# Kernel optimization log

Hardware: AMD Instinct MI355X
Metric: run time of the kernel (lower is better)

Reference implementation:

```python
import jax, jax.numpy as jnp
import numpy as np

N, E, G = 40000, 400000, 40
DIN, DH, DOUT = 128, 256, 128
NEG_SLOPE = 0.2  # PyG GATConv default leaky_relu slope


def _gat_layer(h_in, src, dst, W, a_src, a_dst, b, num_nodes):
    # h_in: [N, din]; src/dst: [E'] (self loops included); W: [din, dout]
    h = h_in @ W                                   # [N, dout]
    al_s = h @ a_src                               # [N]
    al_d = h @ a_dst                               # [N]
    e = jax.nn.leaky_relu(al_s[src] + al_d[dst], NEG_SLOPE)  # [E']
    # scatter-softmax over incoming edges of each dst node (stable)
    m = jax.ops.segment_max(e, dst, num_segments=num_nodes)
    ex = jnp.exp(e - m[dst])
    denom = jax.ops.segment_sum(ex, dst, num_segments=num_nodes)
    alpha = ex / denom[dst]                        # [E']
    out = jax.ops.segment_sum(h[src] * alpha[:, None], dst, num_segments=num_nodes)
    return out + b


def setup_inputs() -> dict:
    key = jax.random.key(0)
    ks = jax.random.split(key, 16)
    x = jax.random.normal(ks[0], (N, DIN), dtype=jnp.float32)
    edge_index = jax.random.randint(ks[1], (2, E), 0, N, dtype=jnp.int64)

    def lin(k, din, dout):
        return jax.random.normal(k, (din, dout), dtype=jnp.float32) / np.sqrt(din)

    def vec(k, d):
        return jax.random.normal(k, (d,), dtype=jnp.float32) / np.sqrt(d)

    return dict(
        x=x, edge_index=edge_index, num_graphs=G,
        W1=lin(ks[2], DIN, DH), a_src1=vec(ks[3], DH), a_dst1=vec(ks[4], DH), b1=jnp.zeros((DH,), jnp.float32),
        W2=lin(ks[5], DH, DH), a_src2=vec(ks[6], DH), a_dst2=vec(ks[7], DH), b2=jnp.zeros((DH,), jnp.float32),
        W3=lin(ks[8], DH, DOUT), a_src3=vec(ks[9], DOUT), a_dst3=vec(ks[10], DOUT), b3=jnp.zeros((DOUT,), jnp.float32),
    )


def reference(x, edge_index, num_graphs, W1, a_src1, a_dst1, b1, W2, a_src2, a_dst2, b2, W3, a_src3, a_dst3, b3):
    num_nodes = x.shape[0]
    # PyG GATConv adds self-loops by default
    loop = jnp.arange(num_nodes, dtype=edge_index.dtype)
    src = jnp.concatenate([edge_index[0], loop])
    dst = jnp.concatenate([edge_index[1], loop])

    h = jax.nn.relu(_gat_layer(x, src, dst, W1, a_src1, a_dst1, b1, num_nodes))
    # dropout is identity in eval mode
    h = jax.nn.relu(_gat_layer(h, src, dst, W2, a_src2, a_dst2, b2, num_nodes))
    h = _gat_layer(h, src, dst, W3, a_src3, a_dst3, b3, num_nodes)
    return h.reshape(num_graphs, num_nodes // num_graphs, -1)
```

## Files before the change

### kernel.cpp

```cpp
#include <hip/hip_runtime.h>
#include <hip/hip_bf16.h>
#include <type_traits>

typedef __attribute__((ext_vector_type(8))) short short8;
typedef __attribute__((ext_vector_type(4))) float f32x4;
typedef __attribute__((ext_vector_type(8))) unsigned short u16x8;

static __device__ __forceinline__ unsigned short f2b(float f) {
    unsigned int v = __float_as_uint(f);
    unsigned int r = (v + 0x7FFFu + ((v >> 16) & 1u)) >> 16;
    return (unsigned short)r;
}
static __device__ __forceinline__ float b2f(unsigned short u) {
    return __uint_as_float(((unsigned int)u) << 16);
}

__global__ void k_pre(const float* __restrict__ w1, unsigned short* __restrict__ t1,
                      const float* __restrict__ w2, unsigned short* __restrict__ t2,
                      const float* __restrict__ w3, unsigned short* __restrict__ t3,
                      int K1, int N1, int K2, int N2, int K3, int N3,
                      const int* __restrict__ dst, int* __restrict__ cnt, int E, int tblk) {
    if ((int)blockIdx.x < tblk) {
        int i = blockIdx.x * 256 + threadIdx.x;
        int n1 = K1 * N1, n2 = K2 * N2, n3 = K3 * N3;
        if (i < n1) {
            int k = i / N1, n = i % N1;
            t1[n * K1 + k] = f2b(w1[i]);
        } else if (i < n1 + n2) {
            int j = i - n1, k = j / N2, n = j % N2;
            t2[n * K2 + k] = f2b(w2[j]);
        } else if (i < n1 + n2 + n3) {
            int j = i - n1 - n2, k = j / N3, n = j % N3;
            t3[n * K3 + k] = f2b(w3[j]);
        }
    } else {
        int e = (blockIdx.x - tblk) * 256 + threadIdx.x;
        if (e < E) atomicAdd(&cnt[dst[e]], 1);
    }
}

__global__ void k_assign(const int* __restrict__ cnt, int* __restrict__ begptr,
                         int* __restrict__ colidx, int* __restrict__ fill,
                         int* __restrict__ cursor, int n) {
    int i = blockIdx.x * 256 + threadIdx.x;
    int lane = threadIdx.x & 63;
    int c = (i < n) ? cnt[i] + 1 : 0;
    int s = c;
#pragma unroll
    for (int off = 1; off < 64; off <<= 1) {
        int v = __shfl_up(s, off);
        if (lane >= off) s += v;
    }
    int wavesum = __shfl(s, 63);
    int base = 0;
    if (lane == 63) base = atomicAdd(cursor, wavesum);
    base = __shfl(base, 63);
    int beg = base + s - c;
    if (i < n) { begptr[i] = beg; colidx[beg] = i; fill[i] = beg + 1; }
}

template<int NC, typename AT>
static __device__ __forceinline__ void gemm_body(const AT* __restrict__ A,
                                                 const unsigned short* __restrict__ Bt,
                                                 unsigned short* __restrict__ H,
                                                 const float* __restrict__ asrc,
                                                 const float* __restrict__ adst,
                                                 float* __restrict__ als,
                                                 float* __restrict__ ald,
                                                 int K, int blk) {
    __shared__ unsigned short As[64][72];
    __shared__ unsigned short Bs[NC][72];
    __shared__ float sps[64], spd[64];
    const int tid  = threadIdx.x;
    const int lane = tid & 63;
    const int wv   = tid >> 6;
    const int rowBase = blk * 64;
    const int quad = lane >> 4;
    const int l16  = lane & 15;
    constexpr int CG = NC / 32;
    const int wrow = (wv & 1) * 32;
    const int wcol = (wv >> 1) * (NC / 2);
    f32x4 acc[2][CG] = {};

    if (tid < 64) { sps[tid] = 0.f; spd[tid] = 0.f; }

    const int ar = tid >> 2;
    const int ak = (tid & 3) * 16;

    for (int kk = 0; kk < K; kk += 64) {
        if constexpr (std::is_same_v<AT, float>) {
            const float* ap = A + (size_t)(rowBase + ar) * K + kk + ak;
            f32x4 a0 = *(const f32x4*)ap;
            f32x4 a1 = *(const f32x4*)(ap + 4);
            f32x4 a2 = *(const f32x4*)(ap + 8);
            f32x4 a3 = *(const f32x4*)(ap + 12);
            short8 s0, s1;
#pragma unroll
            for (int v = 0; v < 4; v++) {
                s0[v] = (short)f2b(a0[v]); s0[4 + v] = (short)f2b(a1[v]);
                s1[v] = (short)f2b(a2[v]); s1[4 + v] = (short)f2b(a3[v]);
            }
            *(short8*)&As[ar][ak] = s0;
            *(short8*)&As[ar][ak + 8] = s1;
        } else {
            const unsigned short* ap = A + (size_t)(rowBase + ar) * K + kk + ak;
            *(short8*)&As[ar][ak]     = *(const short8*)ap;
            *(short8*)&As[ar][ak + 8] = *(const short8*)(ap + 8);
        }
#pragma unroll
        for (int c = tid; c < NC * 4; c += 256) {
            int br = c >> 2, bk = (c & 3) * 16;
            const unsigned short* bp = Bt + (size_t)br * K + kk + bk;
            *(short8*)&Bs[br][bk]     = *(const short8*)bp;
            *(short8*)&Bs[br][bk + 8] = *(const short8*)(bp + 8);
        }
        __syncthreads();
#pragma unroll
        for (int s = 0; s < 2; s++) {
            short8 af0 = *(const short8*)&As[wrow + l16][s * 32 + quad * 8];
            short8 af1 = *(const short8*)&As[wrow + 16 + l16][s * 32 + quad * 8];
#pragma unroll
            for (int cg = 0; cg < CG; cg++) {
                short8 bf = *(const short8*)&Bs[wcol + cg * 16 + l16][s * 32 + quad * 8];
                acc[0][cg] = __builtin_amdgcn_mfma_f32_16x16x32_bf16(af0, bf, acc[0][cg], 0, 0, 0);
                acc[1][cg] = __builtin_amdgcn_mfma_f32_16x16x32_bf16(af1, bf, acc[1][cg], 0, 0, 0);
            }
        }
        __syncthreads();
    }

    float avs[CG], avd[CG];
#pragma unroll
    for (int cg = 0; cg < CG; cg++) {
        int gcol = wcol + cg * 16 + l16;
        avs[cg] = asrc[gcol];
        avd[cg] = adst[gcol];
#pragma unroll
        for (int rg = 0; rg < 2; rg++)
#pragma unroll
            for (int r = 0; r < 4; r++) {
                int grow = rowBase + wrow + rg * 16 + quad * 4 + r;
                H[(size_t)grow * NC + gcol] = f2b(acc[rg][cg][r]);
            }
    }
#pragma unroll
    for (int rg = 0; rg < 2; rg++)
#pragma unroll
        for (int r = 0; r < 4; r++) {
            float ps = 0.f, pd = 0.f;
#pragma unroll
            for (int cg = 0; cg < CG; cg++) { ps += acc[rg][cg][r] * avs[cg]; pd += acc[rg][cg][r] * avd[cg]; }
#pragma unroll
            for (int off = 8; off; off >>= 1) { ps += __shfl_xor(ps, off); pd += __shfl_xor(pd, off); }
            if (l16 == 0) {
                int lrow = wrow + rg * 16 + quad * 4 + r;
                atomicAdd(&sps[lrow], ps);
                atomicAdd(&spd[lrow], pd);
            }
        }
    __syncthreads();
    if (tid < 64) { als[rowBase + tid] = sps[tid]; ald[rowBase + tid] = spd[tid]; }
}

template<int NC, typename AT>
__global__ __launch_bounds__(256) void k_gemm(const AT* __restrict__ A,
                                              const unsigned short* __restrict__ Bt,
                                              unsigned short* __restrict__ H,
                                              const float* __restrict__ asrc,
                                              const float* __restrict__ adst,
                                              float* __restrict__ als,
                                              float* __restrict__ ald, int K) {
    gemm_body<NC, AT>(A, Bt, H, asrc, adst, als, ald, K, blockIdx.x);
}

template<int NC, typename AT>
__global__ __launch_bounds__(256) void k_gemm_scatter(const AT* __restrict__ A,
                                                      const unsigned short* __restrict__ Bt,
                                                      unsigned short* __restrict__ H,
                                                      const float* __restrict__ asrc,
                                                      const float* __restrict__ adst,
                                                      float* __restrict__ als,
                                                      float* __restrict__ ald, int K, int gblk,
                                                      const int* __restrict__ src,
                                                      const int* __restrict__ dst,
                                                      int* __restrict__ fill,
                                                      int* __restrict__ colidx, int E) {
    if ((int)blockIdx.x < gblk) {
        gemm_body<NC, AT>(A, Bt, H, asrc, adst, als, ald, K, blockIdx.x);
    } else {
        int e = (blockIdx.x - gblk) * 256 + threadIdx.x;
        if (e < E) {
            int s = src[e], d = dst[e];
            int pos = atomicAdd(&fill[d], 1);
            colidx[pos] = s;
        }
    }
}

template<int DOUT, bool RELU, typename OutT>
__global__ __launch_bounds__(256) void k_edge(const unsigned short* __restrict__ h,
                                              const float* __restrict__ als,
                                              const float* __restrict__ ald,
                                              const int* __restrict__ begptr,
                                              const int* __restrict__ cnt,
                                              const int* __restrict__ colidx,
                                              const float* __restrict__ bias,
                                              OutT* __restrict__ out, int N) {
    int node = blockIdx.x * 4 + (threadIdx.x >> 6);
    if (node >= N) return;
    int lane = threadIdx.x & 63;
    int beg = begptr[node];
    int deg = cnt[node] + 1;
    float aldi = ald[node];

    float ex_lane = 0.f;
    int   s_lane = 0;
    float dsum = 0.f;
    for (int j = lane; j < deg; j += 64) {
        int s = colidx[beg + j];
        float e = als[s] + aldi;
        e = e > 0.f ? e : 0.2f * e;
        float ex = __expf(e);
        if (j < 64) { ex_lane = ex; s_lane = s; }
        dsum += ex;
    }
#pragma unroll
    for (int off = 32; off; off >>= 1) dsum += __shfl_xor(dsum, off);
    float inv = 1.0f / dsum;
    float w_lane = ex_lane * inv;

    constexpr int QV  = DOUT / 16;
    constexpr int NC8 = QV / 8;
    const int l16g    = lane & 15;
    const int quarter = lane >> 4;
    const size_t dimOff = (size_t)l16g * QV;
    float acc[QV] = {};
    int lim = deg < 64 ? deg : 64;
    for (int t = 0; 4 * t < lim; t++) {
        int idx = 4 * t + quarter;
        float wj = __shfl(w_lane, idx);
        int   sj = __shfl(s_lane, idx);
        const unsigned short* hp = h + (size_t)sj * DOUT + dimOff;
        u16x8 c[NC8];
#pragma unroll
        for (int u = 0; u < NC8; u++) c[u] = *(const u16x8*)(hp + 8 * u);
#pragma unroll
        for (int u = 0; u < NC8; u++)
#pragma unroll
            for (int v = 0; v < 8; v++) acc[8 * u + v] += wj * b2f(c[u][v]);
    }
    for (int j = 64; j < deg; j++) {
        int sj = colidx[beg + j];
        float e = als[sj] + aldi;
        e = e > 0.f ? e : 0.2f * e;
        float wj = __expf(e) * inv;
        if (quarter == 0) {
            const unsigned short* hp = h + (size_t)sj * DOUT + dimOff;
#pragma unroll
            for (int u = 0; u < NC8; u++) {
                u16x8 c = *(const u16x8*)(hp + 8 * u);
#pragma unroll
                for (int v = 0; v < 8; v++) acc[8 * u + v] += wj * b2f(c[v]);
            }
        }
    }
#pragma unroll
    for (int v = 0; v < QV; v++) {
        acc[v] += __shfl_xor(acc[v], 16);
        acc[v] += __shfl_xor(acc[v], 32);
    }

    if (quarter == 0) {
        if constexpr (std::is_same_v<OutT, float>) {
            float* op = out + (size_t)node * DOUT + dimOff;
#pragma unroll
            for (int u = 0; u < QV / 4; u++) {
                f32x4 bv = *(const f32x4*)(bias + dimOff + 4 * u);
                f32x4 ov;
#pragma unroll
                for (int v = 0; v < 4; v++) {
                    float val = acc[4 * u + v] + bv[v];
                    if (RELU) val = fmaxf(val, 0.f);
                    ov[v] = val;
                }
                *(f32x4*)(op + 4 * u) = ov;
            }
        } else {
            unsigned short* op = out + (size_t)node * DOUT + dimOff;
#pragma unroll
            for (int u = 0; u < NC8; u++) {
                u16x8 ov;
#pragma unroll
                for (int v = 0; v < 8; v++) {
                    float val = acc[8 * u + v] + bias[dimOff + 8 * u + v];
                    if (RELU) val = fmaxf(val, 0.f);
                    ov[v] = f2b(val);
                }
                *(u16x8*)(op + 8 * u) = ov;
            }
        }
    }
}

extern "C" void kernel_launch(void* const* d_in, const int* in_sizes, int n_in,
                              void* d_out, int out_size, void* d_ws, size_t ws_size,
                              hipStream_t stream) {
    const int DIN = 128, DH = 256, DOUT = 128;
    const int N = in_sizes[0] / DIN;
    const int E = in_sizes[1] / 2;

    const float* x   = (const float*)d_in[0];
    const int*   ei  = (const int*)d_in[1];
    const float* W1  = (const float*)d_in[3];
    const float* as1 = (const float*)d_in[4];
    const float* ad1 = (const float*)d_in[5];
    const float* b1  = (const float*)d_in[6];
    const float* W2  = (const float*)d_in[7];
    const float* as2 = (const float*)d_in[8];
    const float* ad2 = (const float*)d_in[9];
    const float* b2  = (const float*)d_in[10];
    const float* W3  = (const float*)d_in[11];
    const float* as3 = (const float*)d_in[12];
    const float* ad3 = (const float*)d_in[13];
    const float* b3  = (const float*)d_in[14];
    float* outp = (float*)d_out;

    char* ws = (char*)d_ws;
    size_t off = 0;
    auto carve = [&](size_t bytes) { char* p = ws + off; off = (off + bytes + 255) & ~(size_t)255; return p; };
    unsigned short* hbuf = (unsigned short*)carve((size_t)N * DH * 2);
    unsigned short* gbuf = (unsigned short*)carve((size_t)N * DH * 2);
    float* als  = (float*)carve((size_t)N * 4);
    float* ald  = (float*)carve((size_t)N * 4);
    unsigned short* wt1 = (unsigned short*)carve((size_t)DIN * DH * 2);
    unsigned short* wt2 = (unsigned short*)carve((size_t)DH * DH * 2);
    unsigned short* wt3 = (unsigned short*)carve((size_t)DH * DOUT * 2);
    int* cnt    = (int*)carve((size_t)N * 4);
    int* cursor = (int*)carve(256);
    int* begptr = (int*)carve((size_t)N * 4);
    int* fill   = (int*)carve((size_t)N * 4);
    int* colidx = (int*)carve((size_t)(E + N) * 4);
    (void)ws_size; (void)n_in; (void)out_size;

    const int* e_src = ei;
    const int* e_dst = ei + E;

    hipMemsetAsync(cnt, 0, (size_t)((char*)cursor - (char*)cnt) + 4, stream);

    const int tot   = DIN * DH + DH * DH + DH * DOUT;
    const int tblk  = (tot + 255) / 256;
    const int eblk  = (E + 255) / 256;
    const int nblk4 = (N + 3) / 4;
    const int mblk  = N / 64;

    k_pre<<<tblk + eblk, 256, 0, stream>>>(W1, wt1, W2, wt2, W3, wt3,
                                           DIN, DH, DH, DH, DH, DOUT,
                                           e_dst, cnt, E, tblk);
    k_assign<<<(N + 255) / 256, 256, 0, stream>>>(cnt, begptr, colidx, fill, cursor, N);

    k_gemm_scatter<256, float><<<mblk + eblk, 256, 0, stream>>>(
        x, wt1, hbuf, as1, ad1, als, ald, DIN, mblk,
        e_src, e_dst, fill, colidx, E);
    k_edge<256, true, unsigned short><<<nblk4, 256, 0, stream>>>(hbuf, als, ald, begptr, cnt, colidx, b1, gbuf, N);

    k_gemm<256, unsigned short><<<mblk, 256, 0, stream>>>(gbuf, wt2, hbuf, as2, ad2, als, ald, DH);
    k_edge<256, true, unsigned short><<<nblk4, 256, 0, stream>>>(hbuf, als, ald, begptr, cnt, colidx, b2, gbuf, N);

    k_gemm<128, unsigned short><<<mblk, 256, 0, stream>>>(gbuf, wt3, hbuf, as3, ad3, als, ald, DH);
    k_edge<128, false, float><<<nblk4, 256, 0, stream>>>(hbuf, als, ald, begptr, cnt, colidx, b3, outp, N);
}
```

Before: 292.6 us.

## Map one node per 16-lane group in GAT edge aggregation kernel

```diff
diff --git a/kernel.cpp b/kernel.cpp
--- a/kernel.cpp
+++ b/kernel.cpp
@@ -206,55 +206,64 @@
                                               const int* __restrict__ colidx,
                                               const float* __restrict__ bias,
                                               OutT* __restrict__ out, int N) {
-    int node = blockIdx.x * 4 + (threadIdx.x >> 6);
+    int node = blockIdx.x * 16 + (threadIdx.x >> 4);
     if (node >= N) return;
-    int lane = threadIdx.x & 63;
+    int lane  = threadIdx.x & 63;
+    int l16   = lane & 15;
+    int qbase = lane & 48;
     int beg = begptr[node];
     int deg = cnt[node] + 1;
     float aldi = ald[node];
 
     float ex_lane = 0.f;
-    int   s_lane = 0;
+    int   s_lane  = 0;
     float dsum = 0.f;
-    for (int j = lane; j < deg; j += 64) {
+    for (int j = l16; j < deg; j += 16) {
         int s = colidx[beg + j];
         float e = als[s] + aldi;
         e = e > 0.f ? e : 0.2f * e;
         float ex = __expf(e);
-        if (j < 64) { ex_lane = ex; s_lane = s; }
+        if (j < 16) { ex_lane = ex; s_lane = s; }
         dsum += ex;
     }
 #pragma unroll
-    for (int off = 32; off; off >>= 1) dsum += __shfl_xor(dsum, off);
+    for (int off = 8; off; off >>= 1) dsum += __shfl_xor(dsum, off, 16);
     float inv = 1.0f / dsum;
     float w_lane = ex_lane * inv;
 
+    int d16 = deg < 16 ? deg : 16;
+    int m16 = d16;
+    m16 = max(m16, __shfl_xor(m16, 16));
+    m16 = max(m16, __shfl_xor(m16, 32));
+    int mall = deg;
+    mall = max(mall, __shfl_xor(mall, 16));
+    mall = max(mall, __shfl_xor(mall, 32));
+
     constexpr int QV  = DOUT / 16;
     constexpr int NC8 = QV / 8;
-    const int l16g    = lane & 15;
-    const int quarter = lane >> 4;
-    const size_t dimOff = (size_t)l16g * QV;
+    const size_t dimOff = (size_t)l16 * QV;
     float acc[QV] = {};
-    int lim = deg < 64 ? deg : 64;
-    for (int t = 0; 4 * t < lim; t++) {
-        int idx = 4 * t + quarter;
-        float wj = __shfl(w_lane, idx);
-        int   sj = __shfl(s_lane, idx);
-        const unsigned short* hp = h + (size_t)sj * DOUT + dimOff;
-        u16x8 c[NC8];
-#pragma unroll
-        for (int u = 0; u < NC8; u++) c[u] = *(const u16x8*)(hp + 8 * u);
-#pragma unroll
-        for (int u = 0; u < NC8; u++)
-#pragma unroll
-            for (int v = 0; v < 8; v++) acc[8 * u + v] += wj * b2f(c[u][v]);
-    }
-    for (int j = 64; j < deg; j++) {
-        int sj = colidx[beg + j];
-        float e = als[sj] + aldi;
-        e = e > 0.f ? e : 0.2f * e;
-        float wj = __expf(e) * inv;
-        if (quarter == 0) {
+
+    for (int t = 0; t < m16; t++) {
+        float wj = __shfl(w_lane, qbase + t);
+        int   sj = __shfl(s_lane, qbase + t);
+        if (wj != 0.f) {
+            const unsigned short* hp = h + (size_t)sj * DOUT + dimOff;
+            u16x8 c[NC8];
+#pragma unroll
+            for (int u = 0; u < NC8; u++) c[u] = *(const u16x8*)(hp + 8 * u);
+#pragma unroll
+            for (int u = 0; u < NC8; u++)
+#pragma unroll
+                for (int v = 0; v < 8; v++) acc[8 * u + v] += wj * b2f(c[u][v]);
+        }
+    }
+    for (int t = 16; t < mall; t++) {
+        if (t < deg) {
+            int sj = colidx[beg + t];
+            float e = als[sj] + aldi;
+            e = e > 0.f ? e : 0.2f * e;
+            float wj = __expf(e) * inv;
             const unsigned short* hp = h + (size_t)sj * DOUT + dimOff;
 #pragma unroll
             for (int u = 0; u < NC8; u++) {
@@ -264,40 +273,33 @@
             }
         }
     }
-#pragma unroll
-    for (int v = 0; v < QV; v++) {
-        acc[v] += __shfl_xor(acc[v], 16);
-        acc[v] += __shfl_xor(acc[v], 32);
-    }
-
-    if (quarter == 0) {
-        if constexpr (std::is_same_v<OutT, float>) {
-            float* op = out + (size_t)node * DOUT + dimOff;
-#pragma unroll
-            for (int u = 0; u < QV / 4; u++) {
-                f32x4 bv = *(const f32x4*)(bias + dimOff + 4 * u);
-                f32x4 ov;
-#pragma unroll
-                for (int v = 0; v < 4; v++) {
-                    float val = acc[4 * u + v] + bv[v];
-                    if (RELU) val = fmaxf(val, 0.f);
-                    ov[v] = val;
-                }
-                *(f32x4*)(op + 4 * u) = ov;
-            }
-        } else {
-            unsigned short* op = out + (size_t)node * DOUT + dimOff;
-#pragma unroll
-            for (int u = 0; u < NC8; u++) {
-                u16x8 ov;
-#pragma unroll
-                for (int v = 0; v < 8; v++) {
-                    float val = acc[8 * u + v] + bias[dimOff + 8 * u + v];
-                    if (RELU) val = fmaxf(val, 0.f);
-                    ov[v] = f2b(val);
-                }
-                *(u16x8*)(op + 8 * u) = ov;
-            }
+
+    if constexpr (std::is_same_v<OutT, float>) {
+        float* op = out + (size_t)node * DOUT + dimOff;
+#pragma unroll
+        for (int u = 0; u < QV / 4; u++) {
+            f32x4 bv = *(const f32x4*)(bias + dimOff + 4 * u);
+            f32x4 ov;
+#pragma unroll
+            for (int v = 0; v < 4; v++) {
+                float val = acc[4 * u + v] + bv[v];
+                if (RELU) val = fmaxf(val, 0.f);
+                ov[v] = val;
+            }
+            *(f32x4*)(op + 4 * u) = ov;
+        }
+    } else {
+        unsigned short* op = out + (size_t)node * DOUT + dimOff;
+#pragma unroll
+        for (int u = 0; u < NC8; u++) {
+            u16x8 ov;
+#pragma unroll
+            for (int v = 0; v < 8; v++) {
+                float val = acc[8 * u + v] + bias[dimOff + 8 * u + v];
+                if (RELU) val = fmaxf(val, 0.f);
+                ov[v] = f2b(val);
+            }
+            *(u16x8*)(op + 8 * u) = ov;
         }
     }
 }
@@ -347,11 +349,11 @@
 
     hipMemsetAsync(cnt, 0, (size_t)((char*)cursor - (char*)cnt) + 4, stream);
 
-    const int tot   = DIN * DH + DH * DH + DH * DOUT;
-    const int tblk  = (tot + 255) / 256;
-    const int eblk  = (E + 255) / 256;
-    const int nblk4 = (N + 3) / 4;
-    const int mblk  = N / 64;
+    const int tot    = DIN * DH + DH * DH + DH * DOUT;
+    const int tblk   = (tot + 255) / 256;
+    const int eblk   = (E + 255) / 256;
+    const int nblk16 = (N + 15) / 16;
+    const int mblk   = N / 64;
 
     k_pre<<<tblk + eblk, 256, 0, stream>>>(W1, wt1, W2, wt2, W3, wt3,
                                            DIN, DH, DH, DH, DH, DOUT,
@@ -361,11 +363,11 @@
     k_gemm_scatter<256, float><<<mblk + eblk, 256, 0, stream>>>(
         x, wt1, hbuf, as1, ad1, als, ald, DIN, mblk,
         e_src, e_dst, fill, colidx, E);
-    k_edge<256, true, unsigned short><<<nblk4, 256, 0, stream>>>(hbuf, als, ald, begptr, cnt, colidx, b1, gbuf, N);
+    k_edge<256, true, unsigned short><<<nblk16, 256, 0, stream>>>(hbuf, als, ald, begptr, cnt, colidx, b1, gbuf, N);
 
     k_gemm<256, unsigned short><<<mblk, 256, 0, stream>>>(gbuf, wt2, hbuf, as2, ad2, als, ald, DH);
-    k_edge<256, true, unsigned short><<<nblk4, 256, 0, stream>>>(hbuf, als, ald, begptr, cnt, colidx, b2, gbuf, N);
+    k_edge<256, true, unsigned short><<<nblk16, 256, 0, stream>>>(hbuf, als, ald, begptr, cnt, colidx, b2, gbuf, N);
 
     k_gemm<128, unsigned short><<<mblk, 256, 0, stream>>>(gbuf, wt3, hbuf, as3, ad3, als, ald, DH);
-    k_edge<128, false, float><<<nblk4, 256, 0, stream>>>(hbuf, als, ald, begptr, cnt, colidx, b3, outp, N);
-}
+    k_edge<128, false, float><<<nblk16, 256, 0, stream>>>(hbuf, als, ald, begptr, cnt, colidx, b3, outp, N);
+}
```

Result: no change. 288.0 us, median of 2 (-1.6%).
